# Performance work log

Hardware: AMD Instinct MI355X
Metric: run time of the kernel (lower is better)

## Reference

```python
import jax, jax.numpy as jnp
import numpy as np

D_THRE = 0.1       # compatibility distance threshold
RATIO = 1.0        # fraction of points kept as seeds
NUM_ITERS = 10     # power-iteration steps
NMS_RADIUS = 0.1   # NMS suppression radius
N_PTS = 6144


def _pairwise_dist(p):
    # p: [N, d] -> [N, N] euclidean distance matrix
    diff = p[:, None, :] - p[None, :, :]
    return jnp.linalg.norm(diff, axis=-1)


def setup_inputs() -> dict:
    key = jax.random.key(0)
    k1, k2 = jax.random.split(key)
    ipts2d = jax.random.uniform(k1, (N_PTS, 2), dtype=jnp.float32)
    ipts3d = jax.random.uniform(k2, (N_PTS, 3), dtype=jnp.float32)
    return {"ipts2d": ipts2d, "ipts3d": ipts3d}


def reference(ipts2d, ipts3d):
    N = ipts2d.shape[0]
    p2d_dist = _pairwise_dist(ipts2d)[None]            # [1, N, N]
    p3d_dist = _pairwise_dist(ipts3d)[None]            # [1, N, N]
    cross_dist = jnp.abs(p2d_dist - p3d_dist)          # [1, N, N]
    SC_measure = jnp.clip(1.0 - cross_dist ** 2 / D_THRE ** 2, 0.0, None)
    hard_SC = (cross_dist < D_THRE).astype(jnp.float32)

    # leading eigenvector via power iteration (fixed iteration count;
    # the torch allclose early-exit is a perf shortcut, same math)
    v0 = jnp.ones((1, N, 1), dtype=SC_measure.dtype)

    def body(i, v):
        v = jnp.matmul(SC_measure, v)                  # [1, N, 1]
        return v / (jnp.linalg.norm(v, axis=1, keepdims=True) + 1e-6)

    v = jax.lax.fori_loop(0, NUM_ITERS, body, v0)
    confidence = v[..., 0]                             # [1, N]

    # NMS seed picking (bs = 1)
    scores = confidence
    score_relation = (scores.T >= scores) | (p2d_dist[0] >= NMS_RADIUS)
    is_local_max = jnp.min(score_relation, axis=-1).astype(jnp.float32)
    score_local_max = scores * is_local_max            # [1, N]
    max_num = int(N * RATIO)
    seeds = jnp.argsort(-score_local_max, axis=1)[:, :max_num]  # [1, max_num]

    # seed gather + dense GEMM (computed as in the original; output unused)
    hard_SC_tight = (cross_dist < D_THRE / 2).astype(jnp.float32)
    seed_hard = hard_SC[:, seeds[0], :]                # [1, max_num, N]
    seed_hard_tight = hard_SC_tight[:, seeds[0], :]    # [1, max_num, N]
    SC2_measure = jnp.matmul(seed_hard_tight, hard_SC_tight) * seed_hard
    del SC2_measure  # original discards it and returns confidence

    return confidence
```

## Files before the change

kernel.cpp:

```cpp
#include <hip/hip_runtime.h>

#define NPTS 6144
#define RESCALE (1.0f / 1024.0f)

#define NB   48
#define BT   128
#define NBLK (NB * (NB + 1) / 2)
#define MI   2
#define JT   8
#define ROWU 20
#define OFF_A  0
#define OFF_B  (2 * BT * ROWU)
#define OFF_VJ (4 * BT * ROWU)
#define OFF_VI (4 * BT * ROWU + BT)
#define LDS_U32 (4 * BT * ROWU + 2 * BT)

typedef unsigned short u16;
typedef unsigned int   u32;
typedef float v2f    __attribute__((ext_vector_type(2)));
typedef short bf16x8 __attribute__((ext_vector_type(8)));
typedef float f32x4  __attribute__((ext_vector_type(4)));

__device__ __forceinline__ u16 bsplit(float& x) {
  u32 u = __float_as_uint(x) & 0xFFFF0000u;
  x -= __uint_as_float(u);
  return (u16)(u >> 16);
}
__device__ __forceinline__ u32 pk(u16 lo, u16 hi) { return (u32)lo | ((u32)hi << 16); }

__device__ __forceinline__ void build_i(float x2, float y2, float x3, float y3,
                                        float z3, u32* __restrict__ a2,
                                        u32* __restrict__ a3) {
  float n2 = fmaf(x2, x2, y2 * y2);
  float n3 = fmaf(x3, x3, fmaf(y3, y3, z3 * z3));
  const u16 ONE = 0x3F80;
  float t;
  t = -2.f * x2; u16 AXH = bsplit(t), AXM = bsplit(t), AXL = bsplit(t);
  t = -2.f * y2; u16 AYH = bsplit(t), AYM = bsplit(t), AYL = bsplit(t);
  t = n2;        u16 N2H = bsplit(t), N2M = bsplit(t), N2L = bsplit(t);
  t = -2.f * x3; u16 CXH = bsplit(t), CXM = bsplit(t), CXL = bsplit(t);
  t = -2.f * y3; u16 CYH = bsplit(t), CYM = bsplit(t), CYL = bsplit(t);
  t = -2.f * z3; u16 CZH = bsplit(t), CZM = bsplit(t), CZL = bsplit(t);
  t = n3;        u16 N3H = bsplit(t), N3M = bsplit(t), N3L = bsplit(t);
  a2[0] = pk(AXH, AYH); a2[1] = pk(AXM, AYM); a2[2] = pk(AXH, AYH); a2[3] = pk(AXM, AYM);
  a2[4] = pk(AXL, AYL); a2[5] = pk(AXH, AYH); a2[6] = pk(N2H, N2M); a2[7] = pk(N2L, ONE);
  a2[8] = pk(ONE, ONE);
#pragma unroll
  for (int q = 9; q < 16; ++q) a2[q] = 0u;
  a3[0] = pk(CXH, CYH); a3[1]  = pk(CZH, CXM); a3[2]  = pk(CYM, CZM); a3[3]  = pk(CXH, CYH);
  a3[4] = pk(CZH, CXM); a3[5]  = pk(CYM, CZM); a3[6]  = pk(CXL, CYL); a3[7]  = pk(CZL, CXH);
  a3[8] = pk(CYH, CZH); a3[9]  = pk(N3H, N3M); a3[10] = pk(N3L, ONE); a3[11] = pk(ONE, ONE);
#pragma unroll
  for (int q = 12; q < 16; ++q) a3[q] = 0u;
}

__device__ __forceinline__ void build_j(float x2, float y2, float x3, float y3,
                                        float z3, u32* __restrict__ b2,
                                        u32* __restrict__ b3) {
  float n2 = fmaf(x2, x2, y2 * y2);
  float n3 = fmaf(x3, x3, fmaf(y3, y3, z3 * z3));
  const u16 ONE = 0x3F80;
  float t;
  t = x2; u16 BXH = bsplit(t), BXM = bsplit(t), BXL = bsplit(t);
  t = y2; u16 BYH = bsplit(t), BYM = bsplit(t), BYL = bsplit(t);
  t = n2; u16 N2H = bsplit(t), N2M = bsplit(t), N2L = bsplit(t);
  t = x3; u16 DXH = bsplit(t), DXM = bsplit(t), DXL = bsplit(t);
  t = y3; u16 DYH = bsplit(t), DYM = bsplit(t), DYL = bsplit(t);
  t = z3; u16 DZH = bsplit(t), DZM = bsplit(t), DZL = bsplit(t);
  t = n3; u16 N3H = bsplit(t), N3M = bsplit(t), N3L = bsplit(t);
  b2[0] = pk(BXH, BYH); b2[1] = pk(BXH, BYH); b2[2] = pk(BXM, BYM); b2[3] = pk(BXM, BYM);
  b2[4] = pk(BXH, BYH); b2[5] = pk(BXL, BYL); b2[6] = pk(ONE, ONE); b2[7] = pk(ONE, N2H);
  b2[8] = pk(N2M, N2L);
#pragma unroll
  for (int q = 9; q < 16; ++q) b2[q] = 0u;
  b3[0] = pk(DXH, DYH); b3[1]  = pk(DZH, DXH); b3[2]  = pk(DYH, DZH); b3[3]  = pk(DXM, DYM);
  b3[4] = pk(DZM, DXM); b3[5]  = pk(DYM, DZM); b3[6]  = pk(DXH, DYH); b3[7]  = pk(DZH, DXL);
  b3[8] = pk(DYL, DZL); b3[9]  = pk(ONE, ONE); b3[10] = pk(ONE, N3H); b3[11] = pk(N3M, N3L);
#pragma unroll
  for (int q = 12; q < 16; ++q) b3[q] = 0u;
}

__global__ __launch_bounds__(256) void prep_kernel(float* __restrict__ vA,
                                                   float* __restrict__ vB) {
  int i = blockIdx.x * 256 + threadIdx.x;
  vA[i] = 1.0f;
  vB[i] = 0.0f;
}

__global__ __launch_bounds__(256, 3) void matvec_kernel(
    const float* __restrict__ p2, const float* __restrict__ p3,
    const float* __restrict__ vsrc, float* __restrict__ vdst,
    float* __restrict__ vzero) {
  __shared__ u32 sh[LDS_U32];
  float* shf = (float*)sh;

  int k = blockIdx.x;
  int r = (int)((sqrtf(8.f * (float)k + 1.f) - 1.f) * 0.5f);
  while ((r + 1) * (r + 2) / 2 <= k) ++r;
  while (r * (r + 1) / 2 > k) --r;
  const int ib = k - r * (r + 1) / 2;
  const int jb = r;
  const bool offd = (ib != jb);

  const int t    = threadIdx.x;
  const int lane = t & 63;
  const int wv   = t >> 6;
  const int col  = lane & 15;
  const int kb   = lane >> 4;

  if (t < BT) {
    const int ip = ib * BT + t;
    float x2 = p2[2 * ip], y2 = p2[2 * ip + 1];
    float x3 = p3[3 * ip], y3 = p3[3 * ip + 1], z3 = p3[3 * ip + 2];
    build_i(x2, y2, x3, y3, z3, &sh[OFF_A + t * ROWU],
            &sh[OFF_A + BT * ROWU + t * ROWU]);
    shf[OFF_VI + t] = vsrc[ip];
  } else {
    const int tt = t - BT;
    const int jp = jb * BT + tt;
    float x2 = p2[2 * jp], y2 = p2[2 * jp + 1];
    float x3 = p3[3 * jp], y3 = p3[3 * jp + 1], z3 = p3[3 * jp + 2];
    build_j(x2, y2, x3, y3, z3, &sh[OFF_B + tt * ROWU],
            &sh[OFF_B + BT * ROWU + tt * ROWU]);
    shf[OFF_VJ + tt] = vsrc[jp];
  }
  if (blockIdx.x < 24) vzero[blockIdx.x * 256 + t] = 0.0f;
  __syncthreads();

  bf16x8 a2f[MI], a3f[MI];
  v2f vi2[MI][2];
#pragma unroll
  for (int mi = 0; mi < MI; ++mi) {
    const int rr = wv * 32 + mi * 16 + col;
    a2f[mi] = *(const bf16x8*)&sh[OFF_A + rr * ROWU + kb * 4];
    a3f[mi] = *(const bf16x8*)&sh[OFF_A + BT * ROWU + rr * ROWU + kb * 4];
#pragma unroll
    for (int p = 0; p < 2; ++p) {
      const int re = wv * 32 + mi * 16 + kb * 4 + 2 * p;
      vi2[mi][p] = (v2f){shf[OFF_VI + re], shf[OFF_VI + re + 1]};
    }
  }

  v2f racc[MI][2];
#pragma unroll
  for (int mi = 0; mi < MI; ++mi) {
    racc[mi][0] = (v2f){0.f, 0.f};
    racc[mi][1] = (v2f){0.f, 0.f};
  }
  const v2f kM100 = (v2f){-100.0f, -100.0f};
  const v2f k200  = (v2f){ 200.0f,  200.0f};
  const v2f kOne  = (v2f){   1.0f,    1.0f};
  const v2f kZero = (v2f){   0.0f,    0.0f};
  const f32x4 z4  = (f32x4){0.f, 0.f, 0.f, 0.f};

#pragma unroll
  for (int tj = 0; tj < JT; ++tj) {
    const int jrow = tj * 16 + col;
    const bf16x8 b2f = *(const bf16x8*)&sh[OFF_B + jrow * ROWU + kb * 4];
    const bf16x8 b3f = *(const bf16x8*)&sh[OFF_B + BT * ROWU + jrow * ROWU + kb * 4];
    const float vjs = shf[OFF_VJ + jrow];
    const v2f vj2 = (v2f){vjs, vjs};
    v2f cacc = (v2f){0.f, 0.f};
#pragma unroll
    for (int mi = 0; mi < MI; ++mi) {
      f32x4 aacc = __builtin_amdgcn_mfma_f32_16x16x32_bf16(a2f[mi], b2f, z4, 0, 0, 0);
      f32x4 bacc = __builtin_amdgcn_mfma_f32_16x16x32_bf16(a3f[mi], b3f, z4, 0, 0, 0);
#pragma unroll
      for (int p = 0; p < 2; ++p) {
        v2f a = (v2f){aacc[2 * p], aacc[2 * p + 1]};
        v2f b = (v2f){bacc[2 * p], bacc[2 * p + 1]};
        v2f ab = __builtin_elementwise_max(a * b, kZero);
        v2f s  = (v2f){__builtin_amdgcn_sqrtf(ab.x), __builtin_amdgcn_sqrtf(ab.y)};
        v2f w  = __builtin_elementwise_fma(a + b, kM100, kOne);
        w = __builtin_elementwise_fma(s, k200, w);
        w = __builtin_elementwise_max(w, kZero);
        racc[mi][p] = __builtin_elementwise_fma(w, vj2, racc[mi][p]);
        if (offd) cacc = __builtin_elementwise_fma(w, vi2[mi][p], cacc);
      }
    }
    if (offd) {
      float c = cacc.x + cacc.y;
      c += __shfl_xor(c, 16);
      c += __shfl_xor(c, 32);
      if (lane < 16) atomicAdd(&vdst[jb * BT + tj * 16 + lane], c * RESCALE);
    }
  }

#pragma unroll
  for (int mi = 0; mi < MI; ++mi) {
#pragma unroll
    for (int p = 0; p < 2; ++p) {
      float r0 = racc[mi][p].x, r1 = racc[mi][p].y;
      r0 += __shfl_xor(r0, 1); r0 += __shfl_xor(r0, 2);
      r0 += __shfl_xor(r0, 4); r0 += __shfl_xor(r0, 8);
      r1 += __shfl_xor(r1, 1); r1 += __shfl_xor(r1, 2);
      r1 += __shfl_xor(r1, 4); r1 += __shfl_xor(r1, 8);
      if (col == 0) {
        const int row = ib * BT + wv * 32 + mi * 16 + kb * 4 + 2 * p;
        atomicAdd(&vdst[row],     r0 * RESCALE);
        atomicAdd(&vdst[row + 1], r1 * RESCALE);
      }
    }
  }
}

__global__ __launch_bounds__(256) void finalize_kernel(
    const float* __restrict__ v, float* __restrict__ out) {
  const int tid = threadIdx.x;
  float ss = 0.0f;
  for (int k = tid; k < NPTS; k += 256) {
    float x = v[k];
    ss = fmaf(x, x, ss);
  }
  for (int off = 32; off > 0; off >>= 1) ss += __shfl_down(ss, off, 64);
  __shared__ float wsum[4];
  if ((tid & 63) == 0) wsum[tid >> 6] = ss;
  __syncthreads();
  float tot = wsum[0] + wsum[1] + wsum[2] + wsum[3];
  float inv = 1.0f / (sqrtf(tot) + 1e-6f);
  int i = blockIdx.x * 256 + tid;
  out[i] = v[i] * inv;
}

extern "C" void kernel_launch(void* const* d_in, const int* in_sizes, int n_in,
                              void* d_out, int out_size, void* d_ws, size_t ws_size,
                              hipStream_t stream) {
  const float* p2 = (const float*)d_in[0];
  const float* p3 = (const float*)d_in[1];
  float* out = (float*)d_out;

  float* w = (float*)d_ws;
  float* buf[3] = { w, w + 8192, w + 16384 };

  prep_kernel<<<NPTS / 256, 256, 0, stream>>>(buf[0], buf[1]);

  for (int k = 0; k < 10; ++k) {
    matvec_kernel<<<NBLK, 256, 0, stream>>>(
        p2, p3, buf[k % 3], buf[(k + 1) % 3], buf[(k + 2) % 3]);
  }

  finalize_kernel<<<NPTS / 256, 256, 0, stream>>>(buf[1], out);
}
```

Measured before the change: 227.5 us.

## Fuse power iterations into one persistent kernel with grid barriers

Replaces the ten separate matvec launches plus the finalize launch with a single persistent kernel of 512 blocks. Each block loops over the triangular tiles, and the iterations are separated by an atomic-counter grid barrier; the final normalization also runs inside this kernel. The LDS row stride shrinks from 20 to 12 words, with the padding lanes now reading a shared zero slot. This removes launch overhead and the tail effects between iterations. In exchange it adds spin-wait barrier cost and relies on all 512 blocks being co-resident, which would deadlock if they are not.

```diff
diff --git a/kernel.cpp b/kernel.cpp
--- a/kernel.cpp
+++ b/kernel.cpp
@@ -2,18 +2,22 @@
 
 #define NPTS 6144
 #define RESCALE (1.0f / 1024.0f)
+#define NITER 10
 
 #define NB   48
 #define BT   128
-#define NBLK (NB * (NB + 1) / 2)
+#define NTILE (NB * (NB + 1) / 2)
+#define GRID  512
 #define MI   2
 #define JT   8
-#define ROWU 20
-#define OFF_A  0
-#define OFF_B  (2 * BT * ROWU)
+#define ROWU 12
+#define OFF_A3 (BT * ROWU)
+#define OFF_B2 (2 * BT * ROWU)
+#define OFF_B3 (3 * BT * ROWU)
 #define OFF_VJ (4 * BT * ROWU)
-#define OFF_VI (4 * BT * ROWU + BT)
-#define LDS_U32 (4 * BT * ROWU + 2 * BT)
+#define OFF_VI (OFF_VJ + BT)
+#define OFF_Z  (OFF_VJ + 2 * BT)
+#define LDS_U32 (OFF_Z + 4)
 
 typedef unsigned short u16;
 typedef unsigned int   u32;
@@ -44,14 +48,10 @@
   t = n3;        u16 N3H = bsplit(t), N3M = bsplit(t), N3L = bsplit(t);
   a2[0] = pk(AXH, AYH); a2[1] = pk(AXM, AYM); a2[2] = pk(AXH, AYH); a2[3] = pk(AXM, AYM);
   a2[4] = pk(AXL, AYL); a2[5] = pk(AXH, AYH); a2[6] = pk(N2H, N2M); a2[7] = pk(N2L, ONE);
-  a2[8] = pk(ONE, ONE);
-#pragma unroll
-  for (int q = 9; q < 16; ++q) a2[q] = 0u;
+  a2[8] = pk(ONE, ONE); a2[9] = 0u; a2[10] = 0u; a2[11] = 0u;
   a3[0] = pk(CXH, CYH); a3[1]  = pk(CZH, CXM); a3[2]  = pk(CYM, CZM); a3[3]  = pk(CXH, CYH);
   a3[4] = pk(CZH, CXM); a3[5]  = pk(CYM, CZM); a3[6]  = pk(CXL, CYL); a3[7]  = pk(CZL, CXH);
   a3[8] = pk(CYH, CZH); a3[9]  = pk(N3H, N3M); a3[10] = pk(N3L, ONE); a3[11] = pk(ONE, ONE);
-#pragma unroll
-  for (int q = 12; q < 16; ++q) a3[q] = 0u;
 }
 
 __device__ __forceinline__ void build_j(float x2, float y2, float x3, float y3,
@@ -70,156 +70,183 @@
   t = n3; u16 N3H = bsplit(t), N3M = bsplit(t), N3L = bsplit(t);
   b2[0] = pk(BXH, BYH); b2[1] = pk(BXH, BYH); b2[2] = pk(BXM, BYM); b2[3] = pk(BXM, BYM);
   b2[4] = pk(BXH, BYH); b2[5] = pk(BXL, BYL); b2[6] = pk(ONE, ONE); b2[7] = pk(ONE, N2H);
-  b2[8] = pk(N2M, N2L);
-#pragma unroll
-  for (int q = 9; q < 16; ++q) b2[q] = 0u;
+  b2[8] = pk(N2M, N2L); b2[9] = 0u; b2[10] = 0u; b2[11] = 0u;
   b3[0] = pk(DXH, DYH); b3[1]  = pk(DZH, DXH); b3[2]  = pk(DYH, DZH); b3[3]  = pk(DXM, DYM);
   b3[4] = pk(DZM, DXM); b3[5]  = pk(DYM, DZM); b3[6]  = pk(DXH, DYH); b3[7]  = pk(DZH, DXL);
   b3[8] = pk(DYL, DZL); b3[9]  = pk(ONE, ONE); b3[10] = pk(ONE, N3H); b3[11] = pk(N3M, N3L);
-#pragma unroll
-  for (int q = 12; q < 16; ++q) b3[q] = 0u;
 }
 
 __global__ __launch_bounds__(256) void prep_kernel(float* __restrict__ vA,
-                                                   float* __restrict__ vB) {
+                                                   float* __restrict__ vB,
+                                                   u32* __restrict__ cnt) {
   int i = blockIdx.x * 256 + threadIdx.x;
-  vA[i] = 1.0f;
-  vB[i] = 0.0f;
-}
-
-__global__ __launch_bounds__(256, 3) void matvec_kernel(
+  if (i < NPTS) { vA[i] = 1.0f; vB[i] = 0.0f; }
+  if (blockIdx.x == 0 && threadIdx.x < 16) cnt[threadIdx.x] = 0u;
+}
+
+__device__ __forceinline__ void gbar(u32* __restrict__ c) {
+  __syncthreads();
+  if (threadIdx.x == 0) {
+    __hip_atomic_fetch_add(c, 1u, __ATOMIC_ACQ_REL, __HIP_MEMORY_SCOPE_AGENT);
+    u32 v;
+    do {
+      __builtin_amdgcn_s_sleep(2);
+      v = __hip_atomic_load(c, __ATOMIC_ACQUIRE, __HIP_MEMORY_SCOPE_AGENT);
+    } while (v < (u32)GRID);
+  }
+  __syncthreads();
+  __threadfence();
+}
+
+__global__ __launch_bounds__(256, 2) void sc2_kernel(
     const float* __restrict__ p2, const float* __restrict__ p3,
-    const float* __restrict__ vsrc, float* __restrict__ vdst,
-    float* __restrict__ vzero) {
+    float* __restrict__ b0, float* __restrict__ b1, float* __restrict__ b2v,
+    u32* __restrict__ cnt, float* __restrict__ out) {
   __shared__ u32 sh[LDS_U32];
   float* shf = (float*)sh;
 
-  int k = blockIdx.x;
-  int r = (int)((sqrtf(8.f * (float)k + 1.f) - 1.f) * 0.5f);
-  while ((r + 1) * (r + 2) / 2 <= k) ++r;
-  while (r * (r + 1) / 2 > k) --r;
-  const int ib = k - r * (r + 1) / 2;
-  const int jb = r;
-  const bool offd = (ib != jb);
-
+  const int bid  = blockIdx.x;
   const int t    = threadIdx.x;
   const int lane = t & 63;
   const int wv   = t >> 6;
   const int col  = lane & 15;
   const int kb   = lane >> 4;
-
-  if (t < BT) {
-    const int ip = ib * BT + t;
-    float x2 = p2[2 * ip], y2 = p2[2 * ip + 1];
-    float x3 = p3[3 * ip], y3 = p3[3 * ip + 1], z3 = p3[3 * ip + 2];
-    build_i(x2, y2, x3, y3, z3, &sh[OFF_A + t * ROWU],
-            &sh[OFF_A + BT * ROWU + t * ROWU]);
-    shf[OFF_VI + t] = vsrc[ip];
-  } else {
-    const int tt = t - BT;
-    const int jp = jb * BT + tt;
-    float x2 = p2[2 * jp], y2 = p2[2 * jp + 1];
-    float x3 = p3[3 * jp], y3 = p3[3 * jp + 1], z3 = p3[3 * jp + 2];
-    build_j(x2, y2, x3, y3, z3, &sh[OFF_B + tt * ROWU],
-            &sh[OFF_B + BT * ROWU + tt * ROWU]);
-    shf[OFF_VJ + tt] = vsrc[jp];
-  }
-  if (blockIdx.x < 24) vzero[blockIdx.x * 256 + t] = 0.0f;
-  __syncthreads();
-
-  bf16x8 a2f[MI], a3f[MI];
-  v2f vi2[MI][2];
-#pragma unroll
-  for (int mi = 0; mi < MI; ++mi) {
-    const int rr = wv * 32 + mi * 16 + col;
-    a2f[mi] = *(const bf16x8*)&sh[OFF_A + rr * ROWU + kb * 4];
-    a3f[mi] = *(const bf16x8*)&sh[OFF_A + BT * ROWU + rr * ROWU + kb * 4];
-#pragma unroll
-    for (int p = 0; p < 2; ++p) {
-      const int re = wv * 32 + mi * 16 + kb * 4 + 2 * p;
-      vi2[mi][p] = (v2f){shf[OFF_VI + re], shf[OFF_VI + re + 1]};
-    }
-  }
-
-  v2f racc[MI][2];
-#pragma unroll
-  for (int mi = 0; mi < MI; ++mi) {
-    racc[mi][0] = (v2f){0.f, 0.f};
-    racc[mi][1] = (v2f){0.f, 0.f};
-  }
+  const int kb4  = kb * 4;
+  const bool k3  = (kb == 3);
+
+  if (t < 4) sh[OFF_Z + t] = 0u;
+
   const v2f kM100 = (v2f){-100.0f, -100.0f};
   const v2f k200  = (v2f){ 200.0f,  200.0f};
   const v2f kOne  = (v2f){   1.0f,    1.0f};
   const v2f kZero = (v2f){   0.0f,    0.0f};
   const f32x4 z4  = (f32x4){0.f, 0.f, 0.f, 0.f};
 
-#pragma unroll
-  for (int tj = 0; tj < JT; ++tj) {
-    const int jrow = tj * 16 + col;
-    const bf16x8 b2f = *(const bf16x8*)&sh[OFF_B + jrow * ROWU + kb * 4];
-    const bf16x8 b3f = *(const bf16x8*)&sh[OFF_B + BT * ROWU + jrow * ROWU + kb * 4];
-    const float vjs = shf[OFF_VJ + jrow];
-    const v2f vj2 = (v2f){vjs, vjs};
-    v2f cacc = (v2f){0.f, 0.f};
-#pragma unroll
-    for (int mi = 0; mi < MI; ++mi) {
-      f32x4 aacc = __builtin_amdgcn_mfma_f32_16x16x32_bf16(a2f[mi], b2f, z4, 0, 0, 0);
-      f32x4 bacc = __builtin_amdgcn_mfma_f32_16x16x32_bf16(a3f[mi], b3f, z4, 0, 0, 0);
-#pragma unroll
-      for (int p = 0; p < 2; ++p) {
-        v2f a = (v2f){aacc[2 * p], aacc[2 * p + 1]};
-        v2f b = (v2f){bacc[2 * p], bacc[2 * p + 1]};
-        v2f ab = __builtin_elementwise_max(a * b, kZero);
-        v2f s  = (v2f){__builtin_amdgcn_sqrtf(ab.x), __builtin_amdgcn_sqrtf(ab.y)};
-        v2f w  = __builtin_elementwise_fma(a + b, kM100, kOne);
-        w = __builtin_elementwise_fma(s, k200, w);
-        w = __builtin_elementwise_max(w, kZero);
-        racc[mi][p] = __builtin_elementwise_fma(w, vj2, racc[mi][p]);
-        if (offd) cacc = __builtin_elementwise_fma(w, vi2[mi][p], cacc);
+  float* va = b0;
+  float* vb = b1;
+  float* vc = b2v;
+
+  for (int it = 0; it < NITER; ++it) {
+    const float* vsrc = va;
+    float* vdst = vb;
+    if (bid < NPTS / 256) vc[bid * 256 + t] = 0.0f;
+
+    for (int tl = bid; tl < NTILE; tl += GRID) {
+      int r = (int)((sqrtf(8.f * (float)tl + 1.f) - 1.f) * 0.5f);
+      while ((r + 1) * (r + 2) / 2 <= tl) ++r;
+      while (r * (r + 1) / 2 > tl) --r;
+      const int ib = tl - r * (r + 1) / 2;
+      const int jb = r;
+      const bool offd = (ib != jb);
+
+      __syncthreads();
+      if (t < BT) {
+        const int ip = ib * BT + t;
+        float x2 = p2[2 * ip], y2 = p2[2 * ip + 1];
+        float x3 = p3[3 * ip], y3 = p3[3 * ip + 1], z3 = p3[3 * ip + 2];
+        build_i(x2, y2, x3, y3, z3, &sh[t * ROWU], &sh[OFF_A3 + t * ROWU]);
+        shf[OFF_VI + t] = vsrc[ip];
+      } else {
+        const int tt = t - BT;
+        const int jp = jb * BT + tt;
+        float x2 = p2[2 * jp], y2 = p2[2 * jp + 1];
+        float x3 = p3[3 * jp], y3 = p3[3 * jp + 1], z3 = p3[3 * jp + 2];
+        build_j(x2, y2, x3, y3, z3, &sh[OFF_B2 + tt * ROWU],
+                &sh[OFF_B3 + tt * ROWU]);
+        shf[OFF_VJ + tt] = vsrc[jp];
+      }
+      __syncthreads();
+
+      bf16x8 a2f[MI], a3f[MI];
+      v2f vi2[MI][2];
+#pragma unroll
+      for (int mi = 0; mi < MI; ++mi) {
+        const int rr = wv * 32 + mi * 16 + col;
+        a2f[mi] = *(const bf16x8*)&sh[k3 ? OFF_Z : (rr * ROWU + kb4)];
+        a3f[mi] = *(const bf16x8*)&sh[k3 ? OFF_Z : (OFF_A3 + rr * ROWU + kb4)];
+#pragma unroll
+        for (int p = 0; p < 2; ++p) {
+          const int re = wv * 32 + mi * 16 + kb4 + 2 * p;
+          vi2[mi][p] = (v2f){shf[OFF_VI + re], shf[OFF_VI + re + 1]};
+        }
+      }
+
+      v2f racc[MI][2];
+#pragma unroll
+      for (int mi = 0; mi < MI; ++mi) {
+        racc[mi][0] = (v2f){0.f, 0.f};
+        racc[mi][1] = (v2f){0.f, 0.f};
+      }
+
+#pragma unroll
+      for (int tj = 0; tj < JT; ++tj) {
+        const int jrow = tj * 16 + col;
+        const bf16x8 b2f = *(const bf16x8*)&sh[k3 ? OFF_Z : (OFF_B2 + jrow * ROWU + kb4)];
+        const bf16x8 b3f = *(const bf16x8*)&sh[k3 ? OFF_Z : (OFF_B3 + jrow * ROWU + kb4)];
+        const float vjs = shf[OFF_VJ + jrow];
+        const v2f vj2 = (v2f){vjs, vjs};
+        v2f cacc = (v2f){0.f, 0.f};
+#pragma unroll
+        for (int mi = 0; mi < MI; ++mi) {
+          f32x4 aacc = __builtin_amdgcn_mfma_f32_16x16x32_bf16(a2f[mi], b2f, z4, 0, 0, 0);
+          f32x4 bacc = __builtin_amdgcn_mfma_f32_16x16x32_bf16(a3f[mi], b3f, z4, 0, 0, 0);
+#pragma unroll
+          for (int p = 0; p < 2; ++p) {
+            v2f a = (v2f){aacc[2 * p], aacc[2 * p + 1]};
+            v2f b = (v2f){bacc[2 * p], bacc[2 * p + 1]};
+            v2f ab = __builtin_elementwise_max(a * b, kZero);
+            v2f s  = (v2f){__builtin_amdgcn_sqrtf(ab.x), __builtin_amdgcn_sqrtf(ab.y)};
+            v2f w  = __builtin_elementwise_fma(a + b, kM100, kOne);
+            w = __builtin_elementwise_fma(s, k200, w);
+            w = __builtin_elementwise_max(w, kZero);
+            racc[mi][p] = __builtin_elementwise_fma(w, vj2, racc[mi][p]);
+            if (offd) cacc = __builtin_elementwise_fma(w, vi2[mi][p], cacc);
+          }
+        }
+        if (offd) {
+          float c = cacc.x + cacc.y;
+          c += __shfl_xor(c, 16);
+          c += __shfl_xor(c, 32);
+          if (lane < 16) atomicAdd(&vdst[jb * BT + tj * 16 + lane], c * RESCALE);
+        }
+      }
+
+#pragma unroll
+      for (int mi = 0; mi < MI; ++mi) {
+#pragma unroll
+        for (int p = 0; p < 2; ++p) {
+          float r0 = racc[mi][p].x, r1 = racc[mi][p].y;
+          r0 += __shfl_xor(r0, 1); r0 += __shfl_xor(r0, 2);
+          r0 += __shfl_xor(r0, 4); r0 += __shfl_xor(r0, 8);
+          r1 += __shfl_xor(r1, 1); r1 += __shfl_xor(r1, 2);
+          r1 += __shfl_xor(r1, 4); r1 += __shfl_xor(r1, 8);
+          if (col == 0) {
+            const int row = ib * BT + wv * 32 + mi * 16 + kb4 + 2 * p;
+            atomicAdd(&vdst[row],     r0 * RESCALE);
+            atomicAdd(&vdst[row + 1], r1 * RESCALE);
+          }
+        }
       }
     }
-    if (offd) {
-      float c = cacc.x + cacc.y;
-      c += __shfl_xor(c, 16);
-      c += __shfl_xor(c, 32);
-      if (lane < 16) atomicAdd(&vdst[jb * BT + tj * 16 + lane], c * RESCALE);
+    gbar(&cnt[it]);
+    float* tmp = va; va = vb; vb = vc; vc = tmp;
+  }
+
+  if (bid < NPTS / 256) {
+    float ss = 0.0f;
+    for (int k = t; k < NPTS; k += 256) {
+      float x = va[k];
+      ss = fmaf(x, x, ss);
     }
+    for (int off = 32; off > 0; off >>= 1) ss += __shfl_down(ss, off, 64);
+    __syncthreads();
+    if ((t & 63) == 0) shf[t >> 6] = ss;
+    __syncthreads();
+    float tot = shf[0] + shf[1] + shf[2] + shf[3];
+    float inv = 1.0f / (sqrtf(tot) + 1e-6f);
+    const int i = bid * 256 + t;
+    out[i] = va[i] * inv;
   }
-
-#pragma unroll
-  for (int mi = 0; mi < MI; ++mi) {
-#pragma unroll
-    for (int p = 0; p < 2; ++p) {
-      float r0 = racc[mi][p].x, r1 = racc[mi][p].y;
-      r0 += __shfl_xor(r0, 1); r0 += __shfl_xor(r0, 2);
-      r0 += __shfl_xor(r0, 4); r0 += __shfl_xor(r0, 8);
-      r1 += __shfl_xor(r1, 1); r1 += __shfl_xor(r1, 2);
-      r1 += __shfl_xor(r1, 4); r1 += __shfl_xor(r1, 8);
-      if (col == 0) {
-        const int row = ib * BT + wv * 32 + mi * 16 + kb * 4 + 2 * p;
-        atomicAdd(&vdst[row],     r0 * RESCALE);
-        atomicAdd(&vdst[row + 1], r1 * RESCALE);
-      }
-    }
-  }
-}
-
-__global__ __launch_bounds__(256) void finalize_kernel(
-    const float* __restrict__ v, float* __restrict__ out) {
-  const int tid = threadIdx.x;
-  float ss = 0.0f;
-  for (int k = tid; k < NPTS; k += 256) {
-    float x = v[k];
-    ss = fmaf(x, x, ss);
-  }
-  for (int off = 32; off > 0; off >>= 1) ss += __shfl_down(ss, off, 64);
-  __shared__ float wsum[4];
-  if ((tid & 63) == 0) wsum[tid >> 6] = ss;
-  __syncthreads();
-  float tot = wsum[0] + wsum[1] + wsum[2] + wsum[3];
-  float inv = 1.0f / (sqrtf(tot) + 1e-6f);
-  int i = blockIdx.x * 256 + tid;
-  out[i] = v[i] * inv;
 }
 
 extern "C" void kernel_launch(void* const* d_in, const int* in_sizes, int n_in,
@@ -230,14 +257,11 @@
   float* out = (float*)d_out;
 
   float* w = (float*)d_ws;
-  float* buf[3] = { w, w + 8192, w + 16384 };
-
-  prep_kernel<<<NPTS / 256, 256, 0, stream>>>(buf[0], buf[1]);
-
-  for (int k = 0; k < 10; ++k) {
-    matvec_kernel<<<NBLK, 256, 0, stream>>>(
-        p2, p3, buf[k % 3], buf[(k + 1) % 3], buf[(k + 2) % 3]);
-  }
-
-  finalize_kernel<<<NPTS / 256, 256, 0, stream>>>(buf[1], out);
-}
+  float* b0 = w;
+  float* b1 = w + 8192;
+  float* b2v = w + 16384;
+  u32*   cnt = (u32*)(w + 24576);
+
+  prep_kernel<<<NPTS / 256, 256, 0, stream>>>(b0, b1, cnt);
+  sc2_kernel<<<GRID, 256, 0, stream>>>(p2, p3, b0, b1, b2v, cnt, out);
+}
```

Measured after the change: 850.6 us. 3.74x slower.
